# Performance work log

Measured on AMD Instinct MI355X. Metric: run time of the kernel, lower is better.

Reference implementation:

```python
import jax, jax.numpy as jnp
import numpy as np
from jax import lax


def conv2d_same(x, w):
    # x: [N,C,H,W], w: [O,I,3,3] -> [N,O,H,W], stride 1, padding 1
    return lax.conv_general_dilated(x, w, (1, 1), 'SAME',
                                    dimension_numbers=('NCHW', 'OIHW', 'NCHW'))


def bilinear_gather(x, py, px):
    # x: [N,C,H,W]; py,px: [N,K,H,W] float sampling coords (zero pad outside)
    # returns [N,C,K,H,W]
    N, C, H, W = x.shape
    y0f = jnp.floor(py)
    x0f = jnp.floor(px)
    wy = (py - y0f)[:, None]  # [N,1,K,H,W]
    wx = (px - x0f)[:, None]
    y0 = y0f.astype(jnp.int32)
    x0 = x0f.astype(jnp.int32)
    flat = x.reshape(N, C, H * W)

    def gather(yi, xi):
        valid = ((yi >= 0) & (yi < H) & (xi >= 0) & (xi < W))
        yc = jnp.clip(yi, 0, H - 1)
        xc = jnp.clip(xi, 0, W - 1)
        idx = (yc * W + xc).reshape(N, 1, -1)          # [N,1,K*H*W]
        g = jnp.take_along_axis(flat, jnp.broadcast_to(idx, (N, C, idx.shape[-1])), axis=2)
        g = g.reshape(N, C, *yi.shape[1:])             # [N,C,K,H,W]
        return g * valid.astype(x.dtype)[:, None]

    v00 = gather(y0, x0)
    v01 = gather(y0, x0 + 1)
    v10 = gather(y0 + 1, x0)
    v11 = gather(y0 + 1, x0 + 1)
    return (v00 * (1 - wy) * (1 - wx) + v01 * (1 - wy) * wx
            + v10 * wy * (1 - wx) + v11 * wy * wx)


def deform_conv(x, off, w, b):
    # x: [N,C,H,W]; off: [N,18,H,W] (dy,dx per 3x3 tap); w: [O,C,3,3]; b: [O]
    N, C, H, W = x.shape
    K = 9
    off = off.reshape(N, K, 2, H, W)
    kdy, kdx = jnp.meshgrid(jnp.arange(3) - 1, jnp.arange(3) - 1, indexing='ij')
    kdy = kdy.reshape(K).astype(x.dtype)
    kdx = kdx.reshape(K).astype(x.dtype)
    hh = jnp.arange(H, dtype=x.dtype)
    ww = jnp.arange(W, dtype=x.dtype)
    py = off[:, :, 0] + hh[None, None, :, None] + kdy[None, :, None, None]  # [N,K,H,W]
    px = off[:, :, 1] + ww[None, None, None, :] + kdx[None, :, None, None]
    sampled = bilinear_gather(x, py, px)               # [N,C,K,H,W]
    out = jnp.einsum('nckhw,ock->nohw', sampled, w.reshape(w.shape[0], C, K))
    return out + b[None, :, None, None]


def setup_inputs() -> dict:
    key = jax.random.key(0)
    ks = jax.random.split(key, 8)
    B, obj, C, H, W = 2, 4, 256, 48, 48
    return {
        'query': jax.random.normal(ks[0], (B, C, H, W), jnp.float32),
        'key': jax.random.normal(ks[1], (B, C, H, W), jnp.float32),
        'value': jax.random.normal(ks[2], (B, obj, C, H, W), jnp.float32),
        'off_conv_w': jax.random.normal(ks[3], (C, 2 * C, 3, 3), jnp.float32) * 0.02,
        'off_conv_b': jnp.zeros((C,), jnp.float32),
        'offp_w': jax.random.normal(ks[4], (18, C, 3, 3), jnp.float32) * 0.02,
        'offp_b': jnp.zeros((18,), jnp.float32),
        'deform_w': jax.random.normal(ks[5], (C, C, 3, 3), jnp.float32) * 0.02,
        'deform_b': jnp.zeros((C,), jnp.float32),
    }


def reference(query, key, value, off_conv_w, off_conv_b, offp_w, offp_b, deform_w, deform_b):
    B, obj, C, H, W = value.shape
    N = B * obj
    concat = jnp.concatenate([query, key], axis=1)                    # [B,2C,H,W]
    feat = conv2d_same(concat, off_conv_w) + off_conv_b[None, :, None, None]
    feat = jnp.broadcast_to(feat[:, None], (B, obj, C, H, W)).reshape(N, C, H, W)
    x = value.reshape(N, C, H, W)
    off = conv2d_same(feat, offp_w) + offp_b[None, :, None, None]     # [N,18,H,W]
    out = deform_conv(x, off, deform_w, deform_b)                     # [N,C,H,W]
    out = out.reshape(N, C, H * W).transpose(2, 0, 1)                 # [HW,N,C]
    q = jnp.broadcast_to(query[:, None], (B, obj, C, H, W)).reshape(N, C, H * W)
    return q.transpose(2, 0, 1) + out
```

## Files before the change

### kernel.cpp

```cpp
#include <hip/hip_runtime.h>

#define HH 48
#define WW 48
#define HWP 2304
#define CC 256
#define NB 8
#define QKROW 2305

typedef __attribute__((ext_vector_type(8))) short short8;
typedef __attribute__((ext_vector_type(4))) short bf16x4;
typedef __attribute__((ext_vector_type(4))) float floatx4;

static __device__ __forceinline__ unsigned short f2bf(float f) {
    union { float f; unsigned u; } v; v.f = f;
    unsigned r = v.u + 0x7fffu + ((v.u >> 16) & 1u);
    return (unsigned short)(r >> 16);
}
static __device__ __forceinline__ float bf2f(short v) {
    union { unsigned u; float f; } x; x.u = ((unsigned)(unsigned short)v) << 16;
    return x.f;
}

__global__ __launch_bounds__(256) void k_trprep(const float* __restrict__ q,
        const float* __restrict__ kk, const float* __restrict__ v,
        const float* __restrict__ w1, const float* __restrict__ dw,
        const float* __restrict__ w2, unsigned short* __restrict__ qkT,
        float* __restrict__ qT, unsigned short* __restrict__ vT,
        unsigned short* __restrict__ w1r, unsigned short* __restrict__ wdr,
        unsigned short* __restrict__ w2r, unsigned short* __restrict__ featb) {
    __shared__ float T[64][65];
    const int bid = blockIdx.x;
    if (bid < 7201) {
        if (bid == 7200) {
            int t = threadIdx.x;
#pragma unroll
            for (int b = 0; b < 2; b++) {
                qkT[((size_t)b * QKROW + HWP) * 512 + t] = 0;
                qkT[((size_t)b * QKROW + HWP) * 512 + 256 + t] = 0;
                featb[((size_t)b * QKROW + HWP) * 256 + t] = 0;
            }
            return;
        }
        int idx = bid * 256 + threadIdx.x;
        if (idx < 1179648) {
            int j = idx & 7, l = (idx >> 3) & 63, mtg = (idx >> 9) & 15;
            int kkk = (idx >> 13) & 15, tap = idx >> 17;
            int o = mtg * 16 + (l & 15);
            int c2 = kkk * 32 + (l >> 4) * 8 + j;
            w1r[idx] = f2bf(w1[((size_t)o * 512 + c2) * 9 + tap]);
        } else if (idx < 1179648 + 589824) {
            int i2 = idx - 1179648;
            int j = i2 & 7, l = (i2 >> 3) & 63, mtg = (i2 >> 9) & 15;
            int kkk = (i2 >> 13) & 7, tap = i2 >> 16;
            int o = mtg * 16 + (l & 15);
            int c = kkk * 32 + (l >> 4) * 8 + j;
            wdr[i2] = f2bf(dw[((size_t)o * 256 + c) * 9 + tap]);
        } else {
            int i2 = idx - 1179648 - 589824;
            int j = i2 & 7, l = (i2 >> 3) & 63, mt = (i2 >> 9) & 1;
            int kkk = (i2 >> 10) & 7, tap = i2 >> 13;
            int o = mt * 16 + (l & 15);
            int c = kkk * 32 + (l >> 4) * 8 + j;
            w2r[i2] = (o < 18) ? f2bf(w2[((size_t)o * 256 + c) * 9 + tap]) : 0;
        }
        return;
    }
    const int idx2 = bid - 7201;
    const int pg = idx2 % 36;
    const int rest = idx2 / 36;
    const int cg = rest & 3, z = rest >> 2;
    const int tx = threadIdx.x & 63, ty = threadIdx.x >> 6;
    if (z < 4) {
        const int b = z >> 1, src = z & 1;
        const float* s = (src ? kk : q) + (size_t)b * CC * HWP;
#pragma unroll
        for (int i = 0; i < 16; i++) {
            int cl = ty * 16 + i;
            T[cl][tx] = s[(size_t)(cg * 64 + cl) * HWP + pg * 64 + tx];
        }
        __syncthreads();
#pragma unroll
        for (int i = 0; i < 16; i++) {
            int pxl = ty * 16 + i;
            float val = T[tx][pxl];
            qkT[((size_t)b * QKROW + pg * 64 + pxl) * 512 + src * 256 + cg * 64 + tx]
                = f2bf(val);
            if (src == 0)
                qT[((size_t)(pg * 64 + pxl) * 2 + b) * 256 + cg * 64 + tx] = val;
        }
    } else {
        const int n = z - 4;
        const float* s = v + (size_t)n * CC * HWP;
#pragma unroll
        for (int i = 0; i < 16; i++) {
            int cl = ty * 16 + i;
            T[cl][tx] = s[(size_t)(cg * 64 + cl) * HWP + pg * 64 + tx];
        }
        __syncthreads();
#pragma unroll
        for (int i = 0; i < 16; i++) {
            int pxl = ty * 16 + i;
            vT[((size_t)n * HWP + pg * 64 + pxl) * 256 + cg * 64 + tx] = f2bf(T[tx][pxl]);
        }
    }
}

__global__ __launch_bounds__(512, 4) void k_conv1(const unsigned short* __restrict__ qkT,
        const unsigned short* __restrict__ w1r, const float* __restrict__ b1,
        unsigned short* __restrict__ featb) {
    __shared__ __align__(16) unsigned short Bl[2][32 * 64 * 8];

    const int tid = threadIdx.x;
    const int pt = blockIdx.x;
    const int b  = blockIdx.y;
    const int oh = blockIdx.z;
    const int px0 = pt * 32;
    const int lane = tid & 63, wv = tid >> 6;
    const int lo = lane & 15, quad = lane >> 4;
    const int mtg = oh * 8 + wv;

    floatx4 acc[2];
    acc[0] = (floatx4)0.f; acc[1] = (floatx4)0.f;

    short8 R[4];
    auto stage_load = [&](int tap) {
        const int dy = tap / 3 - 1, dx = tap % 3 - 1;
#pragma unroll
        for (int k = 0; k < 4; k++) {
            int seg = tid + k * 512;
            int cl  = seg >> 6;
            int sl  = seg & 63;
            int px  = px0 + cl;
            int h = px / WW, w = px - (px / WW) * WW;
            bool val = (h + dy >= 0) && (h + dy < HH)
                       && (w + dx >= 0) && (w + dx < WW);
            int row = val ? (px + dy * WW + dx) : HWP;
            R[k] = *(const short8*)(qkT + ((size_t)b * QKROW + row) * 512 + sl * 8);
        }
    };

    stage_load(0);
    int buf = 0;

    for (int tap = 0; tap < 9; tap++) {
        unsigned short* sb = &Bl[buf][0];
#pragma unroll
        for (int k = 0; k < 4; k++) {
            int seg = tid + k * 512;
            int cl = seg >> 6, sl = seg & 63;
            int slw = sl ^ (cl & 7);
            *(short8*)(sb + ((size_t)cl * 64 + slw) * 8) = R[k];
        }
        __syncthreads();

        if (tap < 8) stage_load(tap + 1);

        const unsigned short* afr = w1r + (((size_t)tap * 16 * 16 + mtg) * 64 + lane) * 8;
#pragma unroll 4
        for (int ks = 0; ks < 16; ks++) {
            short8 a = *(const short8*)(afr + (size_t)ks * 16 * 512);
#pragma unroll
            for (int nt = 0; nt < 2; nt++) {
                int cl = nt * 16 + lo;
                int slot = (ks * 4 + quad) ^ (cl & 7);
                short8 bf = *(const short8*)(sb + ((size_t)cl * 64 + slot) * 8);
                acc[nt] = __builtin_amdgcn_mfma_f32_16x16x32_bf16(a, bf, acc[nt], 0, 0, 0);
            }
        }
        buf ^= 1;
    }

    const int o = mtg * 16 + quad * 4;
    const float b0 = b1[o], bb1 = b1[o + 1], bb2 = b1[o + 2], bb3 = b1[o + 3];
#pragma unroll
    for (int nt = 0; nt < 2; nt++) {
        int px = px0 + nt * 16 + lo;
        bf16x4 pk;
        pk[0] = (short)f2bf(acc[nt][0] + b0);
        pk[1] = (short)f2bf(acc[nt][1] + bb1);
        pk[2] = (short)f2bf(acc[nt][2] + bb2);
        pk[3] = (short)f2bf(acc[nt][3] + bb3);
        *(bf16x4*)(featb + ((size_t)b * QKROW + px) * 256 + o) = pk;
    }
}

__global__ __launch_bounds__(512, 2) void k_conv2(const unsigned short* __restrict__ featb,
        const unsigned short* __restrict__ w2r, const float* __restrict__ b2,
        float* __restrict__ off) {
    __shared__ __align__(16) unsigned short Bl[2][64 * 32 * 8];

    const int tid = threadIdx.x;
    const int pt = blockIdx.x;
    const int b  = blockIdx.y;
    const int px0 = pt * 64;
    const int lane = tid & 63, wv = tid >> 6;
    const int lo = lane & 15, quad = lane >> 4;
    const int mtg = wv & 1;
    const int pxb = wv >> 1;

    floatx4 acc = (floatx4)0.f;

    short8 R[4];
    auto stage_load = [&](int tap) {
        const int dy = tap / 3 - 1, dx = tap % 3 - 1;
#pragma unroll
        for (int k = 0; k < 4; k++) {
            int seg = tid + k * 512;
            int cl  = seg >> 5;
            int sl  = seg & 31;
            int px  = px0 + cl;
            int h = px / WW, w = px - (px / WW) * WW;
            bool val = (h + dy >= 0) && (h + dy < HH)
                       && (w + dx >= 0) && (w + dx < WW);
            int row = val ? (px + dy * WW + dx) : HWP;
            R[k] = *(const short8*)(featb + ((size_t)b * QKROW + row) * 256 + sl * 8);
        }
    };

    stage_load(0);
    int buf = 0;

    for (int tap = 0; tap < 9; tap++) {
        unsigned short* sb = &Bl[buf][0];
#pragma unroll
        for (int k = 0; k < 4; k++) {
            int seg = tid + k * 512;
            int cl = seg >> 5, sl = seg & 31;
            int slw = sl ^ (cl & 7);
            *(short8*)(sb + ((size_t)cl * 32 + slw) * 8) = R[k];
        }
        __syncthreads();

        if (tap < 8) stage_load(tap + 1);

#pragma unroll
        for (int ks = 0; ks < 8; ks++) {
            short8 a = *(const short8*)(w2r + ((((size_t)tap * 8 + ks) * 2 + mtg) * 64 + lane) * 8);
            int cl = pxb * 16 + lo;
            int slot = (ks * 4 + quad) ^ (cl & 7);
            short8 bf = *(const short8*)(sb + ((size_t)cl * 32 + slot) * 8);
            acc = __builtin_amdgcn_mfma_f32_16x16x32_bf16(a, bf, acc, 0, 0, 0);
        }
        buf ^= 1;
    }

    const int o = mtg * 16 + quad * 4;
    const int px = px0 + pxb * 16 + lo;
#pragma unroll
    for (int i = 0; i < 4; i++) {
        int oc = o + i;
        if (oc < 18)
            off[((size_t)b * 18 + oc) * HWP + px] = acc[i] + b2[oc];
    }
}

__global__ __launch_bounds__(512, 2) void k_deform(const unsigned short* __restrict__ vT,
        const float* __restrict__ off, const unsigned short* __restrict__ wdr,
        const float* __restrict__ db, const float* __restrict__ qT,
        float* __restrict__ out) {
    __shared__ __align__(16) unsigned short Sl[2][72 * 256];

    const int tid = threadIdx.x;
    const int bid = blockIdx.x;
    const int c0 = (((bid & 7) << 5) + (bid >> 3)) * 72;
    const int lane = tid & 63, wv = tid >> 6;
    const int lo = lane & 15, quad = lane >> 4;
    const int colg = tid >> 5;
    const int slice = tid & 31;
    const bool real4 = (colg < 8);

    int u_pq[5];
    const float* u_off[5];
    const unsigned short* u_vT[5];
#pragma unroll
    for (int u = 0; u < 5; u++) {
        int cl = colg + u * 16;
        int cg = min(c0 + cl, 18431);
        int pq = cg >> 3, n = cg & 7;
        u_pq[u] = pq;
        u_off[u] = off + (size_t)(n >> 2) * 18 * HWP + pq;
        u_vT[u]  = vT + (size_t)n * HWP * 256 + slice * 8;
    }

    floatx4 acc[2][5];
#pragma unroll
    for (int mt = 0; mt < 2; mt++)
#pragma unroll
        for (int nt = 0; nt < 5; nt++) acc[mt][nt] = (floatx4)0.f;

    short8 P[5][4];
    float  cwt[5][4];
    float  ndy[5], ndx[5];

    auto prefetch_off = [&](int tap) {
#pragma unroll
        for (int u = 0; u < 5; u++) {
            if (u < 4 || real4) {
                ndy[u] = u_off[u][(2 * tap) * HWP];
                ndx[u] = u_off[u][(2 * tap + 1) * HWP];
            }
        }
    };

    auto prefetch_body = [&](int tap) {
        const float kdy = (float)(tap / 3 - 1), kdx = (float)(tap % 3 - 1);
#pragma unroll
        for (int u = 0; u < 5; u++) {
            if (u < 4 || real4) {
                int pq = u_pq[u];
                int h = pq / WW, w = pq - (pq / WW) * WW;
                float py = ndy[u] + (float)h + kdy;
                float px = ndx[u] + (float)w + kdx;
                float y0f = floorf(py), x0f = floorf(px);
                int y0 = (int)y0f, x0 = (int)x0f;
                float fy = py - y0f, fx = px - x0f;
                bool y0ok = (y0 >= 0) & (y0 < HH), y1ok = (y0 >= -1) & (y0 < HH - 1);
                bool x0ok = (x0 >= 0) & (x0 < WW), x1ok = (x0 >= -1) & (x0 < WW - 1);
                int y0c = min(max(y0, 0), HH - 1), y1c = min(max(y0 + 1, 0), HH - 1);
                int x0c = min(max(x0, 0), WW - 1), x1c = min(max(x0 + 1, 0), WW - 1);
                const unsigned short* r0 = u_vT[u] + (size_t)(y0c * WW + x0c) * 256;
                const unsigned short* r1 = u_vT[u] + (size_t)(y0c * WW + x1c) * 256;
                const unsigned short* r2 = u_vT[u] + (size_t)(y1c * WW + x0c) * 256;
                const unsigned short* r3 = u_vT[u] + (size_t)(y1c * WW + x1c) * 256;
                cwt[u][0] = (y0ok && x0ok) ? (1.f - fy) * (1.f - fx) : 0.f;
                cwt[u][1] = (y0ok && x1ok) ? (1.f - fy) * fx         : 0.f;
                cwt[u][2] = (y1ok && x0ok) ? fy * (1.f - fx)         : 0.f;
                cwt[u][3] = (y1ok && x1ok) ? fy * fx                 : 0.f;
                P[u][0] = *(const short8*)(r0);
                P[u][1] = *(const short8*)(r1);
                P[u][2] = *(const short8*)(r2);
                P[u][3] = *(const short8*)(r3);
            }
        }
    };

    prefetch_off(0);
    prefetch_body(0);
    int buf = 0;

    for (int tap = 0; tap < 9; tap++) {
        if (tap < 8) prefetch_off(tap + 1);
        unsigned short* sb = &Sl[buf][0];
#pragma unroll
        for (int u = 0; u < 5; u++) {
            if (u < 4 || real4) {
                float w0 = cwt[u][0], w1 = cwt[u][1], w2 = cwt[u][2], w3 = cwt[u][3];
                short8 ov;
#pragma unroll
                for (int j = 0; j < 8; j++) {
                    float s = w0 * bf2f(P[u][0][j]) + w1 * bf2f(P[u][1][j])
                            + w2 * bf2f(P[u][2][j]) + w3 * bf2f(P[u][3][j]);
                    ov[j] = (short)f2bf(s);
                }
                int cl = colg + u * 16;
                int slot = slice ^ (cl & 7);
                *(short8*)(sb + cl * 256 + slot * 8) = ov;
            }
        }
        __syncthreads();

        if (tap < 8) prefetch_body(tap + 1);

        const unsigned short* afr = wdr + (((size_t)tap * 8 * 16 + wv * 2) * 64 + lane) * 8;
#pragma unroll
        for (int ks = 0; ks < 8; ks++) {
            const unsigned short* ak = afr + (size_t)ks * 16 * 512;
            short8 a0 = *(const short8*)(ak);
            short8 a1 = *(const short8*)(ak + 512);
#pragma unroll
            for (int nt = 0; nt < 5; nt++) {
                int cl = nt * 16 + lo;
                int clc = min(cl, 71);
                int slot = (ks * 4 + quad) ^ (clc & 7);
                short8 bf = *(const short8*)(sb + clc * 256 + slot * 8);
                acc[0][nt] = __builtin_amdgcn_mfma_f32_16x16x32_bf16(a0, bf, acc[0][nt], 0, 0, 0);
                acc[1][nt] = __builtin_amdgcn_mfma_f32_16x16x32_bf16(a1, bf, acc[1][nt], 0, 0, 0);
            }
        }
        __syncthreads();
        buf ^= 1;
    }

#pragma unroll
    for (int mt = 0; mt < 2; mt++) {
        int o = wv * 32 + mt * 16 + quad * 4;
        float d0 = db[o], d1 = db[o + 1], d2 = db[o + 2], d3 = db[o + 3];
#pragma unroll
        for (int nt = 0; nt < 5; nt++) {
            int cl = nt * 16 + lo;
            if (cl < 72) {
                int cg = c0 + cl;
                int pq = cg >> 3, b = (cg & 7) >> 2;
                floatx4 qv = *(const floatx4*)(qT + ((size_t)pq * 2 + b) * 256 + o);
                floatx4 r = acc[mt][nt];
                r[0] += d0 + qv[0];
                r[1] += d1 + qv[1];
                r[2] += d2 + qv[2];
                r[3] += d3 + qv[3];
                *(floatx4*)(out + (size_t)cg * CC + o) = r;
            }
        }
    }
}

extern "C" void kernel_launch(void* const* d_in, const int* in_sizes, int n_in,
                              void* d_out, int out_size, void* d_ws, size_t ws_size,
                              hipStream_t stream) {
    const float* q  = (const float*)d_in[0];
    const float* k  = (const float*)d_in[1];
    const float* v  = (const float*)d_in[2];
    const float* w1 = (const float*)d_in[3];
    const float* b1 = (const float*)d_in[4];
    const float* w2 = (const float*)d_in[5];
    const float* b2 = (const float*)d_in[6];
    const float* dw = (const float*)d_in[7];
    const float* db = (const float*)d_in[8];
    float* out = (float*)d_out;

    float* off   = (float*)d_ws;
    float* qT    = off + 82944;
    float* off9  = qT + 3538944;
    unsigned short* qkT   = (unsigned short*)(off9 + 1327104);
    unsigned short* vT    = qkT + 2360320;
    unsigned short* featb = vT + 4718592;
    unsigned short* w1r   = featb + 1180160;
    unsigned short* wdr   = w1r + 1179648;
    unsigned short* w2r   = wdr + 589824;

    hipLaunchKernelGGL(k_trprep,dim3(8929),      dim3(256), 0, stream,
                       q, k, v, w1, dw, w2, qkT, qT, vT, w1r, wdr, w2r, featb);
    hipLaunchKernelGGL(k_conv1, dim3(72, 2, 2),  dim3(512), 0, stream, qkT, w1r, b1, featb);
    hipLaunchKernelGGL(k_conv2, dim3(36, 2),     dim3(512), 0, stream, featb, w2r, b2, off);
    hipLaunchKernelGGL(k_deform,dim3(256),       dim3(512), 0, stream, vT, off, wdr, db, qT, out);
}
```

Measured before the change: 199.8 us.

## Vectorize transpose loads and split offset conv into smaller blocks

The transpose-prep kernel now reads rows of q, k and v with float4 loads instead of scalar loads, which cuts the number of global load instructions. The offset conv kernel (k_conv2) is recast from 72 blocks of 512 threads, each covering 64 pixels, to 288 blocks of 128 threads covering 16 pixels each. This spreads the small conv across more compute units for better occupancy. In exchange, each block reloads the weight fragments for fewer pixels, and the float4 shared-memory writes may cause more bank conflicts.

```diff
diff --git a/kernel.cpp b/kernel.cpp
--- a/kernel.cpp
+++ b/kernel.cpp
@@ -70,13 +70,19 @@
     const int rest = idx2 / 36;
     const int cg = rest & 3, z = rest >> 2;
     const int tx = threadIdx.x & 63, ty = threadIdx.x >> 6;
+    const int t4 = threadIdx.x & 15, r4 = threadIdx.x >> 4;
+    const float* s;
     if (z < 4) {
         const int b = z >> 1, src = z & 1;
-        const float* s = (src ? kk : q) + (size_t)b * CC * HWP;
-#pragma unroll
-        for (int i = 0; i < 16; i++) {
-            int cl = ty * 16 + i;
-            T[cl][tx] = s[(size_t)(cg * 64 + cl) * HWP + pg * 64 + tx];
+        s = (src ? kk : q) + (size_t)b * CC * HWP;
+#pragma unroll
+        for (int i = 0; i < 4; i++) {
+            int cl = i * 16 + r4;
+            float4 val = *(const float4*)(s + (size_t)(cg * 64 + cl) * HWP + pg * 64 + t4 * 4);
+            T[cl][t4 * 4 + 0] = val.x;
+            T[cl][t4 * 4 + 1] = val.y;
+            T[cl][t4 * 4 + 2] = val.z;
+            T[cl][t4 * 4 + 3] = val.w;
         }
         __syncthreads();
 #pragma unroll
@@ -90,11 +96,15 @@
         }
     } else {
         const int n = z - 4;
-        const float* s = v + (size_t)n * CC * HWP;
-#pragma unroll
-        for (int i = 0; i < 16; i++) {
-            int cl = ty * 16 + i;
-            T[cl][tx] = s[(size_t)(cg * 64 + cl) * HWP + pg * 64 + tx];
+        s = v + (size_t)n * CC * HWP;
+#pragma unroll
+        for (int i = 0; i < 4; i++) {
+            int cl = i * 16 + r4;
+            float4 val = *(const float4*)(s + (size_t)(cg * 64 + cl) * HWP + pg * 64 + t4 * 4);
+            T[cl][t4 * 4 + 0] = val.x;
+            T[cl][t4 * 4 + 1] = val.y;
+            T[cl][t4 * 4 + 2] = val.z;
+            T[cl][t4 * 4 + 3] = val.w;
         }
         __syncthreads();
 #pragma unroll
@@ -184,19 +194,18 @@
     }
 }
 
-__global__ __launch_bounds__(512, 2) void k_conv2(const unsigned short* __restrict__ featb,
+__global__ __launch_bounds__(128) void k_conv2(const unsigned short* __restrict__ featb,
         const unsigned short* __restrict__ w2r, const float* __restrict__ b2,
         float* __restrict__ off) {
-    __shared__ __align__(16) unsigned short Bl[2][64 * 32 * 8];
+    __shared__ __align__(16) unsigned short Bl[2][16 * 32 * 8];
 
     const int tid = threadIdx.x;
     const int pt = blockIdx.x;
     const int b  = blockIdx.y;
-    const int px0 = pt * 64;
+    const int px0 = pt * 16;
     const int lane = tid & 63, wv = tid >> 6;
     const int lo = lane & 15, quad = lane >> 4;
-    const int mtg = wv & 1;
-    const int pxb = wv >> 1;
+    const int mtg = wv;
 
     floatx4 acc = (floatx4)0.f;
 
@@ -205,7 +214,7 @@
         const int dy = tap / 3 - 1, dx = tap % 3 - 1;
 #pragma unroll
         for (int k = 0; k < 4; k++) {
-            int seg = tid + k * 512;
+            int seg = tid + k * 128;
             int cl  = seg >> 5;
             int sl  = seg & 31;
             int px  = px0 + cl;
@@ -224,7 +233,7 @@
         unsigned short* sb = &Bl[buf][0];
 #pragma unroll
         for (int k = 0; k < 4; k++) {
-            int seg = tid + k * 512;
+            int seg = tid + k * 128;
             int cl = seg >> 5, sl = seg & 31;
             int slw = sl ^ (cl & 7);
             *(short8*)(sb + ((size_t)cl * 32 + slw) * 8) = R[k];
@@ -236,7 +245,7 @@
 #pragma unroll
         for (int ks = 0; ks < 8; ks++) {
             short8 a = *(const short8*)(w2r + ((((size_t)tap * 8 + ks) * 2 + mtg) * 64 + lane) * 8);
-            int cl = pxb * 16 + lo;
+            int cl = lo;
             int slot = (ks * 4 + quad) ^ (cl & 7);
             short8 bf = *(const short8*)(sb + ((size_t)cl * 32 + slot) * 8);
             acc = __builtin_amdgcn_mfma_f32_16x16x32_bf16(a, bf, acc, 0, 0, 0);
@@ -245,7 +254,7 @@
     }
 
     const int o = mtg * 16 + quad * 4;
-    const int px = px0 + pxb * 16 + lo;
+    const int px = px0 + lo;
 #pragma unroll
     for (int i = 0; i < 4; i++) {
         int oc = o + i;
@@ -430,6 +439,6 @@
     hipLaunchKernelGGL(k_trprep,dim3(8929),      dim3(256), 0, stream,
                        q, k, v, w1, dw, w2, qkT, qT, vT, w1r, wdr, w2r, featb);
     hipLaunchKernelGGL(k_conv1, dim3(72, 2, 2),  dim3(512), 0, stream, qkT, w1r, b1, featb);
-    hipLaunchKernelGGL(k_conv2, dim3(36, 2),     dim3(512), 0, stream, featb, w2r, b2, off);
+    hipLaunchKernelGGL(k_conv2, dim3(144, 2),    dim3(128), 0, stream, featb, w2r, b2, off);
     hipLaunchKernelGGL(k_deform,dim3(256),       dim3(512), 0, stream, vT, off, wdr, db, qT, out);
 }
```

Result: no change. 198.7 us (-0.6%).
